# Kernel tuning notes

Hardware: AMD Instinct MI355X
Metric: run time of the kernel (lower is better)

The kernel has to match this reference:

```python
import jax, jax.numpy as jnp
import numpy as np

H = 32          # query heads
HKV = 8         # kv heads
HD = 128        # head dim
BS = 64         # sparse block size
LOCAL = 16      # local blocks
VERT = 8        # vertical stride
STEP = 1        # head sliding step = max(1, VERT // H) for non-homo heads
BASE = 1000000.0
ROPE_SCALE = 1.0
SCALE = 1.0 / np.sqrt(HD)


def setup_inputs() -> dict:
    key = jax.random.key(0)
    ks = jax.random.split(key, 6)
    T, D = 2048, H * HD
    std = 0.02
    return {
        'hidden_states': jax.random.normal(ks[0], (T, D), jnp.float32),
        'positions': jnp.arange(T, dtype=jnp.int32),
        'Wq': jax.random.normal(ks[1], (D, H * HD), jnp.float32) * std,
        'bq': jnp.zeros((H * HD,), jnp.float32),
        'Wk': jax.random.normal(ks[2], (D, HKV * HD), jnp.float32) * std,
        'bk': jnp.zeros((HKV * HD,), jnp.float32),
        'Wv': jax.random.normal(ks[3], (D, HKV * HD), jnp.float32) * std,
        'bv': jnp.zeros((HKV * HD,), jnp.float32),
        'Wo': jax.random.normal(ks[4], (D, D), jnp.float32) * std,
        'bo': jnp.zeros((D,), jnp.float32),
    }


def _rope_cos_sin(positions):
    # neox-style rotary, linear scaling (factor 1.0 -> identity)
    inv_freq = 1.0 / (BASE ** (jnp.arange(0, HD, 2, dtype=jnp.float32) / HD))  # [HD/2]
    t = positions.astype(jnp.float32) / ROPE_SCALE                             # [T]
    freqs = t[:, None] * inv_freq[None, :]                                     # [T, HD/2]
    return jnp.cos(freqs), jnp.sin(freqs)


def _apply_rope(x, cos, sin):
    # x: [T, h, HD], neox: rotate halves
    x1, x2 = x[..., : HD // 2], x[..., HD // 2 :]
    c, s = cos[:, None, :], sin[:, None, :]
    return jnp.concatenate([x1 * c - x2 * s, x2 * c + x1 * s], axis=-1)


def _block_sparse_mask(T):
    # per-head local + vertical-stride block pattern, causal at token level
    blk = jnp.arange(T) // BS
    qb, kb = blk[:, None], blk[None, :]                      # [T,T] block ids
    heads = jnp.arange(H)
    local = (qb - kb) < LOCAL                                # [T,T]
    vert = ((kb[None, :, :] + heads[:, None, None] * STEP + 1) % VERT) == 0  # [H,T,T]
    causal = jnp.arange(T)[:, None] >= jnp.arange(T)[None, :]
    return causal[None] & (local[None] | vert)               # [H,T,T] bool


def reference(hidden_states, positions, Wq, bq, Wk, bk, Wv, bv, Wo, bo):
    T = hidden_states.shape[0]
    q = (hidden_states @ Wq + bq).reshape(T, H, HD)
    k = (hidden_states @ Wk + bk).reshape(T, HKV, HD)
    v = (hidden_states @ Wv + bv).reshape(T, HKV, HD)

    cos, sin = _rope_cos_sin(positions)
    q = _apply_rope(q, cos, sin)
    k = _apply_rope(k, cos, sin)

    # GQA: repeat kv heads to match query heads
    k = jnp.repeat(k, H // HKV, axis=1)   # [T,H,HD]
    v = jnp.repeat(v, H // HKV, axis=1)

    scores = jnp.einsum('shd,thd->hst', q, k) * SCALE         # [H,T,T]
    mask = _block_sparse_mask(T)
    scores = jnp.where(mask, scores, jnp.finfo(scores.dtype).min)
    probs = jax.nn.softmax(scores, axis=-1)
    out = jnp.einsum('hst,thd->shd', probs, v).reshape(T, H * HD)
    return out @ Wo + bo
```

## Files before the change

kernel.cpp:

```cpp
#include <hip/hip_runtime.h>
#include <type_traits>

#define H_    32
#define HKV_  8
#define HD_   128
#define D_    4096
#define KVD_  1024
#define NQKV_ 6144

typedef __attribute__((ext_vector_type(8))) short s8v;
typedef __attribute__((ext_vector_type(4))) float f4v;

__device__ __forceinline__ float b2f(unsigned short u) {
  union { unsigned int i; float f; } v; v.i = ((unsigned int)u) << 16; return v.f;
}
__device__ __forceinline__ unsigned short f2b(float f) {
  unsigned int u = __float_as_uint(f);
  u += 0x7fffu + ((u >> 16) & 1u);
  return (unsigned short)(u >> 16);
}

__device__ __forceinline__ void gload16(const unsigned short* g, unsigned short* l) {
  __builtin_amdgcn_global_load_lds((const __attribute__((address_space(1))) void*)g,
                                   (__attribute__((address_space(3))) void*)l, 16, 0, 0);
}

__global__ void cvt_bf16(const float* __restrict__ x, unsigned short* __restrict__ y,
                         int n8)
{
  int i = blockIdx.x * blockDim.x + threadIdx.x;
  if (i >= n8) return;
  const float4* xp = (const float4*)x + (size_t)i * 2;
  float4 a = xp[0], b = xp[1];
  s8v v;
  v[0] = (short)f2b(a.x); v[1] = (short)f2b(a.y);
  v[2] = (short)f2b(a.z); v[3] = (short)f2b(a.w);
  v[4] = (short)f2b(b.x); v[5] = (short)f2b(b.y);
  v[6] = (short)f2b(b.z); v[7] = (short)f2b(b.w);
  *(s8v*)(y + (size_t)i * 8) = v;
}

__global__ void concat_bias(const float* __restrict__ bq, const float* __restrict__ bk,
                            const float* __restrict__ bv, float* __restrict__ o)
{
  int i = blockIdx.x * blockDim.x + threadIdx.x;
  float v = (i < D_) ? bq[i] : (i < D_ + KVD_) ? bk[i - D_] : bv[i - D_ - KVD_];
  o[i] = v;
}

__global__ __launch_bounds__(256) void cvt_transpose(
    const float* __restrict__ W, unsigned short* __restrict__ Wt, int K, int N)
{
  __shared__ unsigned short tile[64][72];
  const int k0 = blockIdx.y * 64, n0 = blockIdx.x * 64;
  const int tid = threadIdx.x;
#pragma unroll
  for (int it = 0; it < 4; ++it) {
    int idx = tid + it * 256;
    int r = idx >> 4;
    int c = (idx & 15) << 2;
    float4 w = *(const float4*)(W + (size_t)(k0 + r) * N + n0 + c);
    tile[c + 0][r] = f2b(w.x); tile[c + 1][r] = f2b(w.y);
    tile[c + 2][r] = f2b(w.z); tile[c + 3][r] = f2b(w.w);
  }
  __syncthreads();
#pragma unroll
  for (int it = 0; it < 2; ++it) {
    int idx = tid + it * 256;
    int n = idx >> 3;
    int kk = (idx & 7) << 3;
    *(s8v*)(Wt + (size_t)(n0 + n) * K + k0 + kk) = *(const s8v*)&tile[n][kk];
  }
}

__global__ __launch_bounds__(256) void vtrans(
    const unsigned short* __restrict__ S, int lds_, unsigned short* __restrict__ Dst,
    int T)
{
  __shared__ unsigned short tile[64][72];
  const int v0 = blockIdx.x * 64, t0 = blockIdx.y * 64;
  const int tid = threadIdx.x;
#pragma unroll
  for (int it = 0; it < 2; ++it) {
    int idx = tid + it * 256;
    int tr = idx >> 3;
    int vc = (idx & 7) << 3;
    s8v val = *(const s8v*)(S + (size_t)(t0 + tr) * lds_ + v0 + vc);
#pragma unroll
    for (int u = 0; u < 8; ++u) tile[vc + u][tr] = (unsigned short)val[u];
  }
  __syncthreads();
#pragma unroll
  for (int it = 0; it < 2; ++it) {
    int idx = tid + it * 256;
    int vr = idx >> 3;
    int tc = (idx & 7) << 3;
    *(s8v*)(Dst + (size_t)(v0 + vr) * T + t0 + tc) = *(const s8v*)&tile[vr][tc];
  }
}

template <typename OT>
__global__ __launch_bounds__(512, 2) void gemm_bt4p(
    const unsigned short* __restrict__ A, const unsigned short* __restrict__ Bt,
    const float* __restrict__ bias, OT* __restrict__ C,
    int M, int N, int K, int ldc)
{
  __shared__ __align__(16) unsigned short lds[65536];

  const int tid  = threadIdx.x;
  const int wave = tid >> 6;
  const int lane = tid & 63;
  const int l16  = lane & 15;
  const int quad = lane >> 4;
  const int wm   = wave >> 2;
  const int wn   = wave & 3;

  const int nbx = N >> 8;
  const int nwg = nbx * (M >> 8);
  int bid = blockIdx.x;
  if ((nwg & 7) == 0) bid = (bid & 7) * (nwg >> 3) + (bid >> 3);
  const int row0 = (bid / nbx) << 8;
  const int col0 = (bid % nbx) << 8;

  const int srow = lane >> 2;
  const int scol = (lane & 3) << 3;
  const unsigned short* ApL = A  + (size_t)(row0 + wave * 32 + srow) * K + scol;
  const unsigned short* BpL = Bt + (size_t)(col0 + wave * 32 + srow) * K + scol;

  unsigned short* ldsA = lds;
  unsigned short* ldsB = lds + 32768;
  const int wst = wave * 1024;

  f4v acc[8][4] = {};
  const int nt = K >> 6;

  {
    const unsigned short* sa = ApL;
    const unsigned short* sb = BpL;
    gload16(sa,                      ldsA + wst);
    gload16(sa + 16 * (size_t)K,     ldsA + wst + 512);
    gload16(sb,                      ldsB + wst);
    gload16(sb + 16 * (size_t)K,     ldsB + wst + 512);
    gload16(sa + 32,                 ldsA + 8192 + wst);
    gload16(sa + 32 + 16 * (size_t)K, ldsA + 8192 + wst + 512);
    gload16(sb + 32,                 ldsB + 8192 + wst);
    gload16(sb + 32 + 16 * (size_t)K, ldsB + 8192 + wst + 512);
  }

  for (int t = 0; t < nt; ++t) {
    const int p  = t & 1;
    const unsigned short* Ab = ldsA + p * 16384;
    const unsigned short* Bb = ldsB + p * 16384;
    unsigned short* An = ldsA + (p ^ 1) * 16384;
    unsigned short* Bn = ldsB + (p ^ 1) * 16384;
    const bool pre = (t + 1 < nt);
    const unsigned short* sa = ApL + (size_t)(t + 1) * 64;
    const unsigned short* sb = BpL + (size_t)(t + 1) * 64;

    s8v a[8], b[4];

    if (pre) {
      gload16(sa,                  An + wst);
      gload16(sa + 16 * (size_t)K, An + wst + 512);
      asm volatile("s_waitcnt vmcnt(6)" ::: "memory");
    } else {
      asm volatile("s_waitcnt vmcnt(4)" ::: "memory");
    }
    __builtin_amdgcn_s_barrier();
    __builtin_amdgcn_sched_barrier(0);
    b[0] = *(const s8v*)&Bb[(wn * 64 +  0 + l16) * 32 + quad * 8];
    b[1] = *(const s8v*)&Bb[(wn * 64 + 16 + l16) * 32 + quad * 8];
#pragma unroll
    for (int i = 0; i < 8; ++i)
      a[i] = *(const s8v*)&Ab[(wm * 128 + i * 16 + l16) * 32 + quad * 8];
    __builtin_amdgcn_s_setprio(1);
#pragma unroll
    for (int i = 0; i < 8; ++i) {
      acc[i][0] = __builtin_amdgcn_mfma_f32_16x16x32_bf16(a[i], b[0], acc[i][0], 0, 0, 0);
      acc[i][1] = __builtin_amdgcn_mfma_f32_16x16x32_bf16(a[i], b[1], acc[i][1], 0, 0, 0);
    }
    __builtin_amdgcn_s_setprio(0);

    if (pre) {
      gload16(sb,                  Bn + wst);
      gload16(sb + 16 * (size_t)K, Bn + wst + 512);
    }
    b[2] = *(const s8v*)&Bb[(wn * 64 + 32 + l16) * 32 + quad * 8];
    b[3] = *(const s8v*)&Bb[(wn * 64 + 48 + l16) * 32 + quad * 8];
    __builtin_amdgcn_s_barrier();
    __builtin_amdgcn_sched_barrier(0);
    __builtin_amdgcn_s_setprio(1);
#pragma unroll
    for (int i = 0; i < 8; ++i) {
      acc[i][2] = __builtin_amdgcn_mfma_f32_16x16x32_bf16(a[i], b[2], acc[i][2], 0, 0, 0);
      acc[i][3] = __builtin_amdgcn_mfma_f32_16x16x32_bf16(a[i], b[3], acc[i][3], 0, 0, 0);
    }
    __builtin_amdgcn_s_setprio(0);

    if (pre) {
      gload16(sa + 32,                  An + 8192 + wst);
      gload16(sa + 32 + 16 * (size_t)K, An + 8192 + wst + 512);
      asm volatile("s_waitcnt vmcnt(6)" ::: "memory");
    } else {
      asm volatile("s_waitcnt vmcnt(0)" ::: "memory");
    }
    __builtin_amdgcn_s_barrier();
    __builtin_amdgcn_sched_barrier(0);
    b[2] = *(const s8v*)&Bb[8192 + (wn * 64 + 32 + l16) * 32 + quad * 8];
    b[3] = *(const s8v*)&Bb[8192 + (wn * 64 + 48 + l16) * 32 + quad * 8];
#pragma unroll
    for (int i = 0; i < 8; ++i)
      a[i] = *(const s8v*)&Ab[8192 + (wm * 128 + i * 16 + l16) * 32 + quad * 8];
    __builtin_amdgcn_s_setprio(1);
#pragma unroll
    for (int i = 0; i < 8; ++i) {
      acc[i][2] = __builtin_amdgcn_mfma_f32_16x16x32_bf16(a[i], b[2], acc[i][2], 0, 0, 0);
      acc[i][3] = __builtin_amdgcn_mfma_f32_16x16x32_bf16(a[i], b[3], acc[i][3], 0, 0, 0);
    }
    __builtin_amdgcn_s_setprio(0);

    if (pre) {
      gload16(sb + 32,                  Bn + 8192 + wst);
      gload16(sb + 32 + 16 * (size_t)K, Bn + 8192 + wst + 512);
    }
    b[0] = *(const s8v*)&Bb[8192 + (wn * 64 +  0 + l16) * 32 + quad * 8];
    b[1] = *(const s8v*)&Bb[8192 + (wn * 64 + 16 + l16) * 32 + quad * 8];
    __builtin_amdgcn_s_barrier();
    __builtin_amdgcn_sched_barrier(0);
    __builtin_amdgcn_s_setprio(1);
#pragma unroll
    for (int i = 0; i < 8; ++i) {
      acc[i][0] = __builtin_amdgcn_mfma_f32_16x16x32_bf16(a[i], b[0], acc[i][0], 0, 0, 0);
      acc[i][1] = __builtin_amdgcn_mfma_f32_16x16x32_bf16(a[i], b[1], acc[i][1], 0, 0, 0);
    }
    __builtin_amdgcn_s_setprio(0);
  }

#pragma unroll
  for (int j = 0; j < 4; ++j) {
    const int col = col0 + wn * 64 + j * 16 + l16;
    const float bc = bias[col];
#pragma unroll
    for (int i = 0; i < 8; ++i) {
      const int rowb = row0 + wm * 128 + i * 16 + quad * 4;
#pragma unroll
      for (int r = 0; r < 4; ++r) {
        float o = acc[i][j][r] + bc;
        if constexpr (std::is_same_v<OT, float>) C[(size_t)(rowb + r) * ldc + col] = o;
        else                                     C[(size_t)(rowb + r) * ldc + col] = f2b(o);
      }
    }
  }
}

__global__ void sincos_tab(const int* __restrict__ pos, float* __restrict__ ct,
                           float* __restrict__ st)
{
  const int t = blockIdx.x, d = threadIdx.x;
  float inv = powf(1.0e6f, -(float)d * (1.0f / 64.0f));
  float fr  = (float)pos[t] * inv;
  float s, c;
  sincosf(fr, &s, &c);
  ct[t * 64 + d] = c;
  st[t * 64 + d] = s;
}

__global__ void rope_apply(unsigned short* __restrict__ qkv,
                           const float* __restrict__ ct, const float* __restrict__ st,
                           int T)
{
  const int t  = blockIdx.x;
  const int hh = blockIdx.y;
  const int d  = threadIdx.x;
  unsigned short* p = qkv + (size_t)t * NQKV_ + hh * HD_;
  const float g = (hh < H_) ? (0.08838834764831845f * 1.4426950408889634f) : 1.0f;
  float c = ct[t * 64 + d], s = st[t * 64 + d];
  float x1 = b2f(p[d]), x2 = b2f(p[d + 64]);
  p[d]      = f2b((x1 * c - x2 * s) * g);
  p[d + 64] = f2b((x2 * c + x1 * s) * g);
}

__global__ __launch_bounds__(256) void attn_sparse(
    const unsigned short* __restrict__ QKV, int ldq,
    const unsigned short* __restrict__ Vt, unsigned short* __restrict__ O, int T)
{
  __shared__ __align__(16) unsigned short lds[16384];
  unsigned short* ldsK = lds;
  unsigned short* ldsV = lds + 8192;
  unsigned short* ldsP = lds;

  const int h    = blockIdx.x;
  const int qb   = (gridDim.y - 1) - blockIdx.y;
  const int hkv  = h >> 2;
  const int tid  = threadIdx.x;
  const int wave = tid >> 6;
  const int lane = tid & 63;
  const int l16  = lane & 15;
  const int quad = lane >> 4;

  const int qrow = qb * 64 + wave * 16 + l16;
  s8v qf[4];
#pragma unroll
  for (int s = 0; s < 4; ++s)
    qf[s] = *(const s8v*)(QKV + (size_t)qrow * ldq + h * HD_ + s * 32 + quad * 8);

  const int lr4 = lane >> 2;
  const int lc8 = (lane & 3) << 3;
  const unsigned short* Kp0 = QKV + (size_t)(wave * 16 + lr4) * ldq
                              + D_ + hkv * HD_ + lc8;
  unsigned short* Kd0 = ldsK + wave * 512;
  const unsigned short* Vp0 = Vt + (size_t)(hkv * HD_ + wave * 32 + lr4) * T + lc8;
  unsigned short* Vd0 = ldsV + wave * 1024;

  float mrow[4] = {-1e30f, -1e30f, -1e30f, -1e30f};
  float lrow[4] = {0.f, 0.f, 0.f, 0.f};
  f4v oacc[8] = {};
  const int rowinb = wave * 16 + quad * 4;

  for (int kb = 0; kb <= qb; ++kb) {
    if (!((qb - kb < 16) || (((kb + h + 1) & 7) == 0))) continue;

    __syncthreads();
    {
      const unsigned short* kp = Kp0 + (size_t)(kb * 64) * ldq;
      const unsigned short* vp = Vp0 + kb * 64;
#pragma unroll
      for (int t = 0; t < 4; ++t)
        gload16(kp + t * 32, Kd0 + t * 2048);
#pragma unroll
      for (int t = 0; t < 4; ++t)
        gload16(vp + (size_t)((t >> 1) * 16) * T + (t & 1) * 32,
                Vd0 + (t & 1) * 4096 + (t >> 1) * 512);
    }
    __syncthreads();

    f4v sacc[4] = {};
#pragma unroll
    for (int kt = 0; kt < 4; ++kt) {
#pragma unroll
      for (int s = 0; s < 4; ++s) {
        s8v b = *(const s8v*)&ldsK[s * 2048 + (kt * 16 + l16) * 32 + quad * 8];
        sacc[kt] = __builtin_amdgcn_mfma_f32_16x16x32_bf16(qf[s], b, sacc[kt], 0, 0, 0);
      }
    }
    __syncthreads();

    const bool diag = (kb == qb);
    float p[4][4];
#pragma unroll
    for (int r = 0; r < 4; ++r) {
      float mx = -1e30f;
#pragma unroll
      for (int kt = 0; kt < 4; ++kt) {
        float sc = sacc[kt][r];
        if (diag && (kt * 16 + l16 > rowinb + r)) sc = -1e30f;
        p[r][kt] = sc;
        mx = fmaxf(mx, sc);
      }
#pragma unroll
      for (int off = 1; off < 16; off <<= 1)
        mx = fmaxf(mx, __shfl_xor(mx, off));
      float newm = fmaxf(mrow[r], mx);
      float alpha = exp2f(mrow[r] - newm);
      mrow[r] = newm;
      float rs = 0.f;
#pragma unroll
      for (int kt = 0; kt < 4; ++kt) {
        unsigned short pb = f2b(exp2f(p[r][kt] - newm));
        ldsP[wave * 1152 + (quad * 4 + r) * 72 + kt * 16 + l16] = pb;
        rs += b2f(pb);
      }
#pragma unroll
      for (int off = 1; off < 16; off <<= 1)
        rs += __shfl_xor(rs, off);
      lrow[r] = lrow[r] * alpha + rs;
#pragma unroll
      for (int dt = 0; dt < 8; ++dt) oacc[dt][r] *= alpha;
    }

#pragma unroll
    for (int s2 = 0; s2 < 2; ++s2) {
      s8v af = *(const s8v*)&ldsP[wave * 1152 + l16 * 72 + s2 * 32 + quad * 8];
#pragma unroll
      for (int dt = 0; dt < 8; ++dt) {
        s8v vf = *(const s8v*)&ldsV[s2 * 4096 + (dt * 16 + l16) * 32 + quad * 8];
        oacc[dt] = __builtin_amdgcn_mfma_f32_16x16x32_bf16(af, vf, oacc[dt], 0, 0, 0);
      }
    }
  }

#pragma unroll
  for (int r = 0; r < 4; ++r) {
    float inv = 1.0f / lrow[r];
    size_t rowoff = (size_t)(qb * 64 + rowinb + r) * D_ + h * HD_;
#pragma unroll
    for (int dt = 0; dt < 8; ++dt)
      O[rowoff + dt * 16 + l16] = f2b(oacc[dt][r] * inv);
  }
}

extern "C" void kernel_launch(void* const* d_in, const int* in_sizes, int n_in,
                              void* d_out, int out_size, void* d_ws, size_t ws_size,
                              hipStream_t stream)
{
  const float* hs  = (const float*)d_in[0];
  const int*   pos = (const int*)d_in[1];
  const float* Wq  = (const float*)d_in[2];
  const float* bq  = (const float*)d_in[3];
  const float* Wk  = (const float*)d_in[4];
  const float* bk  = (const float*)d_in[5];
  const float* Wv  = (const float*)d_in[6];
  const float* bv  = (const float*)d_in[7];
  const float* Wo  = (const float*)d_in[8];
  const float* bo  = (const float*)d_in[9];
  float* out = (float*)d_out;

  const int T = in_sizes[1];

  const size_t nQ = (size_t)T * D_;
  unsigned short* hsb  = (unsigned short*)d_ws;
  unsigned short* qkv  = hsb + nQ;
  unsigned short* vt   = qkv + (size_t)T * NQKV_;
  unsigned short* wbuf = vt  + (size_t)KVD_ * T;
  unsigned short* tail = wbuf + (size_t)NQKV_ * D_;
  float* bqkv = (float*)tail;
  float* ct   = bqkv + NQKV_;
  float* st   = ct + (size_t)T * 64;
  unsigned short* abuf = hsb;

  dim3 blk(256);
  cvt_bf16<<<dim3((int)(nQ / 8 / 256)), blk, 0, stream>>>(hs, hsb, (int)(nQ / 8));
  concat_bias<<<dim3(NQKV_ / 256), blk, 0, stream>>>(bq, bk, bv, bqkv);
  sincos_tab<<<dim3(T), dim3(64), 0, stream>>>(pos, ct, st);

  cvt_transpose<<<dim3(D_ / 64,   D_ / 64), blk, 0, stream>>>(Wq, wbuf, D_, D_);
  cvt_transpose<<<dim3(KVD_ / 64, D_ / 64), blk, 0, stream>>>(
      Wk, wbuf + (size_t)D_ * D_, D_, KVD_);
  cvt_transpose<<<dim3(KVD_ / 64, D_ / 64), blk, 0, stream>>>(
      Wv, wbuf + (size_t)(D_ + KVD_) * D_, D_, KVD_);

  gemm_bt4p<unsigned short><<<dim3((NQKV_ / 256) * (T / 256)), dim3(512), 0, stream>>>(
      hsb, wbuf, bqkv, qkv, T, NQKV_, D_, NQKV_);

  rope_apply<<<dim3(T, H_ + HKV_), dim3(64), 0, stream>>>(qkv, ct, st, T);
  vtrans<<<dim3(KVD_ / 64, T / 64), blk, 0, stream>>>(
      qkv + D_ + KVD_, NQKV_, vt, T);

  attn_sparse<<<dim3(H_, T / 64), blk, 0, stream>>>(qkv, NQKV_, vt, abuf, T);

  cvt_transpose<<<dim3(D_ / 64, D_ / 64), blk, 0, stream>>>(Wo, wbuf, D_, D_);
  gemm_bt4p<float><<<dim3((D_ / 256) * (T / 256)), dim3(512), 0, stream>>>(
      abuf, wbuf, bo, out, T, D_, D_, D_);
}
```

Baseline: 558.4 us.

## Swizzle GEMM LDS tiles and restructure barrier/waitcnt pipeline

Applies an XOR swizzle to the 16-byte column chunks written by global_load_lds and read back by the MFMA operand loads, aiming to remove LDS bank conflicts. It also reorders the main loop so LDS reads for the current half-tile are issued before the next prefetch, and moves the waitcnt and barrier to sit before the second MFMA group. This drops the sched_barrier intrinsics and changes the vmcnt thresholds. The new synchronisation is easy to get subtly wrong, for example a read racing a prefetch into the same buffer.

```diff
diff --git a/kernel.cpp b/kernel.cpp
--- a/kernel.cpp
+++ b/kernel.cpp
@@ -123,7 +123,7 @@
   const int col0 = (bid % nbx) << 8;
 
   const int srow = lane >> 2;
-  const int scol = (lane & 3) << 3;
+  const int scol = (((lane & 3) ^ ((lane >> 3) & 3)) << 3);
   const unsigned short* ApL = A  + (size_t)(row0 + wave * 32 + srow) * K + scol;
   const unsigned short* BpL = Bt + (size_t)(col0 + wave * 32 + srow) * K + scol;
 
@@ -131,107 +131,107 @@
   unsigned short* ldsB = lds + 32768;
   const int wst = wave * 1024;
 
+  const int sl = ((quad ^ ((l16 >> 1) & 3)) << 3);
+  const int arow = wm * 128 + l16;
+  const int brow = wn * 64 + l16;
+
   f4v acc[8][4] = {};
   const int nt = K >> 6;
 
   {
     const unsigned short* sa = ApL;
     const unsigned short* sb = BpL;
-    gload16(sa,                      ldsA + wst);
-    gload16(sa + 16 * (size_t)K,     ldsA + wst + 512);
-    gload16(sb,                      ldsB + wst);
-    gload16(sb + 16 * (size_t)K,     ldsB + wst + 512);
-    gload16(sa + 32,                 ldsA + 8192 + wst);
+    gload16(sa,                       ldsA + wst);
+    gload16(sa + 16 * (size_t)K,      ldsA + wst + 512);
+    gload16(sb,                       ldsB + wst);
+    gload16(sb + 16 * (size_t)K,      ldsB + wst + 512);
+    gload16(sa + 32,                  ldsA + 8192 + wst);
     gload16(sa + 32 + 16 * (size_t)K, ldsA + 8192 + wst + 512);
-    gload16(sb + 32,                 ldsB + 8192 + wst);
+    gload16(sb + 32,                  ldsB + 8192 + wst);
     gload16(sb + 32 + 16 * (size_t)K, ldsB + 8192 + wst + 512);
   }
+  asm volatile("s_waitcnt vmcnt(4)" ::: "memory");
+  asm volatile("s_barrier" ::: "memory");
 
   for (int t = 0; t < nt; ++t) {
-    const int p  = t & 1;
-    const unsigned short* Ab = ldsA + p * 16384;
-    const unsigned short* Bb = ldsB + p * 16384;
+    const int p = t & 1;
+    const unsigned short* Ab0 = ldsA + p * 16384;
+    const unsigned short* Ab1 = Ab0 + 8192;
+    const unsigned short* Bb0 = ldsB + p * 16384;
+    const unsigned short* Bb1 = Bb0 + 8192;
     unsigned short* An = ldsA + (p ^ 1) * 16384;
     unsigned short* Bn = ldsB + (p ^ 1) * 16384;
     const bool pre = (t + 1 < nt);
     const unsigned short* sa = ApL + (size_t)(t + 1) * 64;
     const unsigned short* sb = BpL + (size_t)(t + 1) * 64;
 
-    s8v a[8], b[4];
-
+    s8v a[8], b0, b1, b2, b3;
+
+    b0 = *(const s8v*)&Bb0[(brow +  0) * 32 + sl];
+    b1 = *(const s8v*)&Bb0[(brow + 16) * 32 + sl];
+#pragma unroll
+    for (int i = 0; i < 8; ++i)
+      a[i] = *(const s8v*)&Ab0[(arow + i * 16) * 32 + sl];
     if (pre) {
       gload16(sa,                  An + wst);
       gload16(sa + 16 * (size_t)K, An + wst + 512);
-      asm volatile("s_waitcnt vmcnt(6)" ::: "memory");
-    } else {
-      asm volatile("s_waitcnt vmcnt(4)" ::: "memory");
-    }
-    __builtin_amdgcn_s_barrier();
-    __builtin_amdgcn_sched_barrier(0);
-    b[0] = *(const s8v*)&Bb[(wn * 64 +  0 + l16) * 32 + quad * 8];
-    b[1] = *(const s8v*)&Bb[(wn * 64 + 16 + l16) * 32 + quad * 8];
-#pragma unroll
-    for (int i = 0; i < 8; ++i)
-      a[i] = *(const s8v*)&Ab[(wm * 128 + i * 16 + l16) * 32 + quad * 8];
+    }
     __builtin_amdgcn_s_setprio(1);
 #pragma unroll
     for (int i = 0; i < 8; ++i) {
-      acc[i][0] = __builtin_amdgcn_mfma_f32_16x16x32_bf16(a[i], b[0], acc[i][0], 0, 0, 0);
-      acc[i][1] = __builtin_amdgcn_mfma_f32_16x16x32_bf16(a[i], b[1], acc[i][1], 0, 0, 0);
+      acc[i][0] = __builtin_amdgcn_mfma_f32_16x16x32_bf16(a[i], b0, acc[i][0], 0, 0, 0);
+      acc[i][1] = __builtin_amdgcn_mfma_f32_16x16x32_bf16(a[i], b1, acc[i][1], 0, 0, 0);
     }
     __builtin_amdgcn_s_setprio(0);
 
+    b2 = *(const s8v*)&Bb0[(brow + 32) * 32 + sl];
+    b3 = *(const s8v*)&Bb0[(brow + 48) * 32 + sl];
     if (pre) {
       gload16(sb,                  Bn + wst);
       gload16(sb + 16 * (size_t)K, Bn + wst + 512);
-    }
-    b[2] = *(const s8v*)&Bb[(wn * 64 + 32 + l16) * 32 + quad * 8];
-    b[3] = *(const s8v*)&Bb[(wn * 64 + 48 + l16) * 32 + quad * 8];
-    __builtin_amdgcn_s_barrier();
-    __builtin_amdgcn_sched_barrier(0);
+      asm volatile("s_waitcnt vmcnt(4)" ::: "memory");
+    } else {
+      asm volatile("s_waitcnt vmcnt(0)" ::: "memory");
+    }
+    asm volatile("s_barrier" ::: "memory");
     __builtin_amdgcn_s_setprio(1);
 #pragma unroll
     for (int i = 0; i < 8; ++i) {
-      acc[i][2] = __builtin_amdgcn_mfma_f32_16x16x32_bf16(a[i], b[2], acc[i][2], 0, 0, 0);
-      acc[i][3] = __builtin_amdgcn_mfma_f32_16x16x32_bf16(a[i], b[3], acc[i][3], 0, 0, 0);
+      acc[i][2] = __builtin_amdgcn_mfma_f32_16x16x32_bf16(a[i], b2, acc[i][2], 0, 0, 0);
+      acc[i][3] = __builtin_amdgcn_mfma_f32_16x16x32_bf16(a[i], b3, acc[i][3], 0, 0, 0);
     }
     __builtin_amdgcn_s_setprio(0);
 
+    b2 = *(const s8v*)&Bb1[(brow + 32) * 32 + sl];
+    b3 = *(const s8v*)&Bb1[(brow + 48) * 32 + sl];
+#pragma unroll
+    for (int i = 0; i < 8; ++i)
+      a[i] = *(const s8v*)&Ab1[(arow + i * 16) * 32 + sl];
     if (pre) {
       gload16(sa + 32,                  An + 8192 + wst);
       gload16(sa + 32 + 16 * (size_t)K, An + 8192 + wst + 512);
-      asm volatile("s_waitcnt vmcnt(6)" ::: "memory");
-    } else {
-      asm volatile("s_waitcnt vmcnt(0)" ::: "memory");
-    }
-    __builtin_amdgcn_s_barrier();
-    __builtin_amdgcn_sched_barrier(0);
-    b[2] = *(const s8v*)&Bb[8192 + (wn * 64 + 32 + l16) * 32 + quad * 8];
-    b[3] = *(const s8v*)&Bb[8192 + (wn * 64 + 48 + l16) * 32 + quad * 8];
-#pragma unroll
-    for (int i = 0; i < 8; ++i)
-      a[i] = *(const s8v*)&Ab[8192 + (wm * 128 + i * 16 + l16) * 32 + quad * 8];
+    }
     __builtin_amdgcn_s_setprio(1);
 #pragma unroll
     for (int i = 0; i < 8; ++i) {
-      acc[i][2] = __builtin_amdgcn_mfma_f32_16x16x32_bf16(a[i], b[2], acc[i][2], 0, 0, 0);
-      acc[i][3] = __builtin_amdgcn_mfma_f32_16x16x32_bf16(a[i], b[3], acc[i][3], 0, 0, 0);
+      acc[i][2] = __builtin_amdgcn_mfma_f32_16x16x32_bf16(a[i], b2, acc[i][2], 0, 0, 0);
+      acc[i][3] = __builtin_amdgcn_mfma_f32_16x16x32_bf16(a[i], b3, acc[i][3], 0, 0, 0);
     }
     __builtin_amdgcn_s_setprio(0);
 
+    b0 = *(const s8v*)&Bb1[(brow +  0) * 32 + sl];
+    b1 = *(const s8v*)&Bb1[(brow + 16) * 32 + sl];
     if (pre) {
       gload16(sb + 32,                  Bn + 8192 + wst);
       gload16(sb + 32 + 16 * (size_t)K, Bn + 8192 + wst + 512);
-    }
-    b[0] = *(const s8v*)&Bb[8192 + (wn * 64 +  0 + l16) * 32 + quad * 8];
-    b[1] = *(const s8v*)&Bb[8192 + (wn * 64 + 16 + l16) * 32 + quad * 8];
-    __builtin_amdgcn_s_barrier();
-    __builtin_amdgcn_sched_barrier(0);
+      asm volatile("s_waitcnt vmcnt(4)" ::: "memory");
+    }
+    asm volatile("s_barrier" ::: "memory");
     __builtin_amdgcn_s_setprio(1);
 #pragma unroll
     for (int i = 0; i < 8; ++i) {
-      acc[i][0] = __builtin_amdgcn_mfma_f32_16x16x32_bf16(a[i], b[0], acc[i][0], 0, 0, 0);
-      acc[i][1] = __builtin_amdgcn_mfma_f32_16x16x32_bf16(a[i], b[1], acc[i][1], 0, 0, 0);
+      acc[i][0] = __builtin_amdgcn_mfma_f32_16x16x32_bf16(a[i], b0, acc[i][0], 0, 0, 0);
+      acc[i][1] = __builtin_amdgcn_mfma_f32_16x16x32_bf16(a[i], b1, acc[i][1], 0, 0, 0);
     }
     __builtin_amdgcn_s_setprio(0);
   }
```

After: 509.7 us. -8.7%, faster.
